# Kernel tuning notes

Measured on AMD Instinct MI355X. Metric: run time of the kernel, lower is better.

The kernel has to match this reference:

```python
import jax, jax.numpy as jnp
import numpy as np

CONF_THRESH = 0.3
NMS_THRESH = 0.5
TOP_K = 64
VAR = (0.1, 0.2)  # standard SSD decode variances


def setup_inputs() -> dict:
    key = jax.random.key(0)
    k1, k2, k3 = jax.random.split(key, 3)
    B, A, C = 16, 16384, 81
    loc = jax.random.normal(k1, (B, A, 4), jnp.float32)
    conf = jax.random.normal(k2, (B, A, C), jnp.float32)
    anchors = jax.random.uniform(k3, (A, 4), jnp.float32)  # cxcywh in [0,1]
    return {"loc": loc, "conf": conf, "anchors": anchors}


def _decode(loc, anchors):
    # SSD-style decode: loc [A,4] offsets, anchors [A,4] cxcywh -> corners [A,4]
    cxcy = anchors[:, :2] + loc[:, :2] * VAR[0] * anchors[:, 2:]
    wh = anchors[:, 2:] * jnp.exp(loc[:, 2:] * VAR[1])
    tl = cxcy - wh * 0.5
    return jnp.concatenate([tl, tl + wh], axis=1)


def _iou(box, boxes):
    # box [4], boxes [A,4] in corner format
    tl = jnp.maximum(box[:2], boxes[:, :2])
    br = jnp.minimum(box[2:], boxes[:, 2:])
    wh = jnp.clip(br - tl, 0.0)
    inter = wh[:, 0] * wh[:, 1]
    a1 = (box[2] - box[0]) * (box[3] - box[1])
    a2 = (boxes[:, 2] - boxes[:, 0]) * (boxes[:, 3] - boxes[:, 1])
    return inter / (a1 + a2 - inter)


def _nms(boxes, scores):
    # greedy NMS for one (batch, class) lane; boxes [A,4], scores [A]
    s0 = jnp.where(scores > CONF_THRESH, scores, -1.0)

    def step(s, _):
        i = jnp.argmax(s)
        sc = s[i]
        box = boxes[i]
        keep = sc > 0.0  # -1 means masked/suppressed; valid scores > conf_thresh > 0
        supp = jnp.where(_iou(box, boxes) > NMS_THRESH, -1.0, s).at[i].set(-1.0)
        s_next = jnp.where(keep, supp, s)
        row = jnp.where(keep, jnp.concatenate([sc[None], box]),
                        jnp.zeros((5,), s.dtype))
        return s_next, row

    _, rows = jax.lax.scan(step, s0, None, length=TOP_K)
    return rows  # [TOP_K, 5] = (score, x1, y1, x2, y2), zero-padded


def reference(loc, conf, anchors):
    conf = jax.nn.sigmoid(conf)                      # [B,A,C]
    boxes = jax.vmap(_decode, in_axes=(0, None))(loc, anchors)  # [B,A,4]
    scores = jnp.swapaxes(conf, 1, 2)                # [B,C,A]
    per_class = jax.vmap(_nms, in_axes=(None, 0))    # over classes
    out = jax.vmap(per_class)(boxes, scores)         # [B,C,TOP_K,5]
    return out
```

## Files before the change

### kernel.cpp

```cpp
#include <hip/hip_runtime.h>
#include <math.h>

constexpr int B_N  = 16;
constexpr int A_N  = 16384;
constexpr int C_N  = 81;
constexpr int TOPK = 64;
constexpr int DNT  = 256;
constexpr int NBINS = 232;
constexpr int CAP   = 512;
constexpr unsigned BIN_BASE = 0x3E99u;

constexpr int TA   = 64;
constexpr int TNT  = 256;
constexpr int TILE_ELEMS = TA * C_N;

__global__ __launch_bounds__(DNT) void decode_kernel(const float4* __restrict__ loc,
                                                     const float4* __restrict__ anch,
                                                     float4* __restrict__ boxes) {
    int i = blockIdx.x * DNT + threadIdx.x;
    int a = i & (A_N - 1);
    float4 l  = loc[i];
    float4 an = anch[a];
    float cx = an.x + (l.x * 0.1f) * an.z;
    float cy = an.y + (l.y * 0.1f) * an.w;
    float w  = an.z * expf(l.z * 0.2f);
    float h  = an.w * expf(l.w * 0.2f);
    float x1 = cx - w * 0.5f;
    float y1 = cy - h * 0.5f;
    boxes[i] = make_float4(x1, y1, x1 + w, y1 + h);
}

__global__ __launch_bounds__(TNT) void sigT_kernel(const float* __restrict__ conf,
                                                   float* __restrict__ scoresT) {
    __shared__ float tile[C_N][TA + 1];

    const int a0 = blockIdx.x * TA;
    const int b  = blockIdx.y;
    const int t  = threadIdx.x;

    const float* src = conf + ((size_t)b * A_N + a0) * C_N;
#pragma unroll
    for (int i = 0; i < (TILE_ELEMS + TNT - 1) / TNT; ++i) {
        int idx = i * TNT + t;
        if (idx < TILE_ELEMS) {
            float x = src[idx];
            int al = idx / C_N;
            int cc = idx - al * C_N;
            tile[cc][al] = 1.0f / (1.0f + expf(-x));
        }
    }
    __syncthreads();
    float* dst = scoresT + (size_t)b * C_N * A_N + a0;
#pragma unroll
    for (int i = 0; i < (TILE_ELEMS + TNT - 1) / TNT; ++i) {
        int idx = i * TNT + t;
        if (idx < TILE_ELEMS) {
            int cc = idx >> 6;
            int al = idx & (TA - 1);
            dst[(size_t)cc * A_N + al] = tile[cc][al];
        }
    }
}

template <bool TRANSPOSED>
__global__ __launch_bounds__(64, 4) void nms_kernel(const float* __restrict__ conf,
                                                    const float* __restrict__ scoresT,
                                                    const float4* __restrict__ boxes,
                                                    float* __restrict__ out) {
    __shared__ int hist[NBINS];
    __shared__ unsigned long long cand[CAP];
    __shared__ int s_cnt;

    const int c    = blockIdx.x;
    const int b    = blockIdx.y;
    const int lane = threadIdx.x;

    for (int i = lane; i < NBINS; i += 64) hist[i] = 0;
    __syncthreads();

    const float4* bptr = boxes + (size_t)b * A_N;
    const float4* sptr = (const float4*)(scoresT + ((size_t)b * C_N + c) * A_N);
    const float*  cptr = conf + (size_t)b * A_N * C_N + c;
    float* optr = out + ((size_t)(b * C_N + c)) * TOPK * 5;

    for (int i = 0; i < A_N / 256; ++i) {
        float s[4];
        if (TRANSPOSED) {
            float4 s4 = sptr[lane + 64 * i];
            s[0] = s4.x; s[1] = s4.y; s[2] = s4.z; s[3] = s4.w;
        } else {
            int a0 = 4 * (lane + 64 * i);
#pragma unroll
            for (int q = 0; q < 4; ++q) {
                float x = cptr[(size_t)(a0 + q) * C_N];
                s[q] = 1.0f / (1.0f + expf(-x));
            }
        }
#pragma unroll
        for (int q = 0; q < 4; ++q) {
            if (s[q] > 0.3f) {
                unsigned u = __float_as_uint(s[q]);
                int bin = (int)(u >> 16) - (int)BIN_BASE;
                bin = bin < 0 ? 0 : (bin > NBINS - 1 ? NBINS - 1 : bin);
                atomicAdd(&hist[bin], 1);
            }
        }
    }
    __syncthreads();

    float rx1 = 0.f, ry1 = 0.f, rx2 = 0.f, ry2 = 0.f, rar = 0.f;
    int acc = 0, kout = 0;

    int bin_hi = NBINS;
    for (;;) {
        int lo = bin_hi, tot = 0;
        while (lo > 0) {
            int cnt = hist[lo - 1];
            if (tot + cnt > CAP) {
                if (tot == 0) { lo--; }
                break;
            }
            tot += cnt; lo--;
        }
        const int bin_lo = lo;
        if (bin_lo == bin_hi) break;
        if (lane == 0) s_cnt = 0;
        __syncthreads();

        for (int i = 0; i < A_N / 256; ++i) {
            float s[4];
            if (TRANSPOSED) {
                float4 s4 = sptr[lane + 64 * i];
                s[0] = s4.x; s[1] = s4.y; s[2] = s4.z; s[3] = s4.w;
            } else {
                int a0 = 4 * (lane + 64 * i);
#pragma unroll
                for (int q = 0; q < 4; ++q) {
                    float x = cptr[(size_t)(a0 + q) * C_N];
                    s[q] = 1.0f / (1.0f + expf(-x));
                }
            }
#pragma unroll
            for (int q = 0; q < 4; ++q) {
                if (s[q] > 0.3f) {
                    unsigned u = __float_as_uint(s[q]);
                    int bin = (int)(u >> 16) - (int)BIN_BASE;
                    bin = bin < 0 ? 0 : (bin > NBINS - 1 ? NBINS - 1 : bin);
                    if (bin >= bin_lo && bin < bin_hi) {
                        int slot = atomicAdd(&s_cnt, 1);
                        if (slot < CAP) {
                            unsigned a = (unsigned)(4 * (lane + 64 * i) + q);
                            cand[slot] = ((unsigned long long)u << 32) | (unsigned)(~a);
                        }
                    }
                }
            }
        }
        __syncthreads();
        int C = s_cnt; if (C > CAP) C = CAP;

        if (C > 0) {
            unsigned long long key[8];
#pragma unroll
            for (int r = 0; r < 8; ++r) {
                int sidx = r * 64 + lane;
                key[r] = (sidx < C) ? cand[sidx] : 0ull;
            }
#pragma unroll
            for (int k = 2; k <= CAP; k <<= 1) {
#pragma unroll
                for (int j = k >> 1; j > 0; j >>= 1) {
                    if (j >= 64) {
                        int jr = j >> 6;
#pragma unroll
                        for (int r = 0; r < 8; ++r) {
                            int rp = r ^ jr;
                            if (rp > r) {
                                int e = r * 64 + lane;
                                bool up = ((e & k) == 0);
                                unsigned long long va = key[r], vb = key[rp];
                                bool sw = up ? (va < vb) : (va > vb);
                                if (sw) { key[r] = vb; key[rp] = va; }
                            }
                        }
                    } else {
#pragma unroll
                        for (int r = 0; r < 8; ++r) {
                            int e = r * 64 + lane;
                            bool up    = ((e & k) == 0);
                            bool isLow = ((lane & j) == 0);
                            unsigned long long va = key[r];
                            unsigned long long vb = __shfl_xor(va, j, 64);
                            bool keepMax = (up == isLow);
                            key[r] = keepMax ? (va > vb ? va : vb)
                                             : (va < vb ? va : vb);
                        }
                    }
                }
            }
            __syncthreads();
#pragma unroll
            for (int r = 0; r < 8; ++r) cand[r * 64 + lane] = key[r];
            __syncthreads();

            int t = 0;
            unsigned long long k0 = cand[0];
            float4 cb = bptr[(int)(~(unsigned)k0)];
            while (t < C) {
                unsigned long long nk = 0ull;
                float4 nb = cb;
                if (t + 1 < C) {
                    nk = cand[t + 1];
                    nb = bptr[(int)(~(unsigned)nk)];
                }
                float sc = __uint_as_float((unsigned)(k0 >> 32));
                float ca = (cb.z - cb.x) * (cb.w - cb.y);
                bool over = false;
                if (lane < acc) {
                    float tlx = fmaxf(rx1, cb.x);
                    float tly = fmaxf(ry1, cb.y);
                    float brx = fminf(rx2, cb.z);
                    float bry = fminf(ry2, cb.w);
                    float iw  = fmaxf(brx - tlx, 0.0f);
                    float ih  = fmaxf(bry - tly, 0.0f);
                    float inter = iw * ih;
                    float iou = inter / (rar + ca - inter);
                    over = iou > 0.5f;
                }
                if (!__any(over)) {
                    if (lane == acc) { rx1 = cb.x; ry1 = cb.y; rx2 = cb.z; ry2 = cb.w; rar = ca; }
                    if (lane == 0) {
                        float* o = optr + (size_t)kout * 5;
                        o[0] = sc; o[1] = cb.x; o[2] = cb.y; o[3] = cb.z; o[4] = cb.w;
                    }
                    acc++; kout++;
                    if (acc == TOPK) break;
                }
                ++t; k0 = nk; cb = nb;
            }
        }
        if (acc == TOPK) break;
        bin_hi = bin_lo;
    }

    {
        float* o  = optr + (size_t)kout * 5;
        int   rem = (TOPK - kout) * 5;
        for (int t = lane; t < rem; t += 64) o[t] = 0.0f;
    }
}

extern "C" void kernel_launch(void* const* d_in, const int* in_sizes, int n_in,
                              void* d_out, int out_size, void* d_ws, size_t ws_size,
                              hipStream_t stream) {
    const float* loc     = (const float*)d_in[0];
    const float* conf    = (const float*)d_in[1];
    const float* anchors = (const float*)d_in[2];
    float* out = (float*)d_out;

    const size_t boxes_bytes  = (size_t)B_N * A_N * sizeof(float4);
    const size_t scores_bytes = (size_t)B_N * C_N * A_N * sizeof(float);

    float4* boxes = (float4*)d_ws;

    decode_kernel<<<(B_N * A_N) / DNT, DNT, 0, stream>>>(
        (const float4*)loc, (const float4*)anchors, boxes);

    if (ws_size >= boxes_bytes + scores_bytes) {
        float* scoresT = (float*)((char*)d_ws + boxes_bytes);
        sigT_kernel<<<dim3(A_N / TA, B_N), TNT, 0, stream>>>(conf, scoresT);
        nms_kernel<true><<<dim3(C_N, B_N), 64, 0, stream>>>(conf, scoresT, boxes, out);
    } else {
        nms_kernel<false><<<dim3(C_N, B_N), 64, 0, stream>>>(conf, nullptr, boxes, out);
    }
}
```

Measured before the change: 267.5 us.

## Split histogram into separate wide kernel, vectorize transpose stores, stage candidate boxes in LDS

Moves the per-(batch,class) score histogram out of the 64-thread NMS kernel into its own 256-thread kernel that writes histograms to workspace, so the scan over 16K scores runs with more parallelism. The transpose kernel now uses a 128-anchor tile stored anchor-major with padding and writes float4 stores. The NMS kernel gathers candidate boxes into shared memory in parallel before the serial greedy loop, so that loop no longer waits on a dependent global load each step. This costs an extra kernel launch, a global histogram round trip and more LDS per block, and the fast path now also needs workspace room for the histograms.

Result: faster. 254.3 us (-4.9%).

```diff
diff --git a/kernel.cpp b/kernel.cpp
--- a/kernel.cpp
+++ b/kernel.cpp
@@ -10,9 +10,13 @@
 constexpr int CAP   = 512;
 constexpr unsigned BIN_BASE = 0x3E99u;
 
-constexpr int TA   = 64;
+constexpr int TA   = 128;
+constexpr int TPAD = 85;
 constexpr int TNT  = 256;
 constexpr int TILE_ELEMS = TA * C_N;
+constexpr int TILE_F4    = (TA / 4) * C_N;
+
+constexpr int HNT = 256;
 
 __global__ __launch_bounds__(DNT) void decode_kernel(const float4* __restrict__ loc,
                                                      const float4* __restrict__ anch,
@@ -32,7 +36,7 @@
 
 __global__ __launch_bounds__(TNT) void sigT_kernel(const float* __restrict__ conf,
                                                    float* __restrict__ scoresT) {
-    __shared__ float tile[C_N][TA + 1];
+    __shared__ float tile[TA][TPAD];
 
     const int a0 = blockIdx.x * TA;
     const int b  = blockIdx.y;
@@ -43,59 +47,41 @@
     for (int i = 0; i < (TILE_ELEMS + TNT - 1) / TNT; ++i) {
         int idx = i * TNT + t;
         if (idx < TILE_ELEMS) {
-            float x = src[idx];
-            int al = idx / C_N;
-            int cc = idx - al * C_N;
-            tile[cc][al] = 1.0f / (1.0f + expf(-x));
+            float x  = src[idx];
+            int   al = idx / C_N;
+            int   cc = idx - al * C_N;
+            tile[al][cc] = 1.0f / (1.0f + expf(-x));
         }
     }
     __syncthreads();
     float* dst = scoresT + (size_t)b * C_N * A_N + a0;
 #pragma unroll
-    for (int i = 0; i < (TILE_ELEMS + TNT - 1) / TNT; ++i) {
-        int idx = i * TNT + t;
-        if (idx < TILE_ELEMS) {
-            int cc = idx >> 6;
-            int al = idx & (TA - 1);
-            dst[(size_t)cc * A_N + al] = tile[cc][al];
-        }
-    }
-}
-
-template <bool TRANSPOSED>
-__global__ __launch_bounds__(64, 4) void nms_kernel(const float* __restrict__ conf,
-                                                    const float* __restrict__ scoresT,
-                                                    const float4* __restrict__ boxes,
-                                                    float* __restrict__ out) {
+    for (int i = 0; i < (TILE_F4 + TNT - 1) / TNT; ++i) {
+        int idx4 = i * TNT + t;
+        if (idx4 < TILE_F4) {
+            int cc  = idx4 >> 5;
+            int al4 = idx4 & 31;
+            float4 v;
+            v.x = tile[al4 * 4 + 0][cc];
+            v.y = tile[al4 * 4 + 1][cc];
+            v.z = tile[al4 * 4 + 2][cc];
+            v.w = tile[al4 * 4 + 3][cc];
+            ((float4*)(dst + (size_t)cc * A_N))[al4] = v;
+        }
+    }
+}
+
+__global__ __launch_bounds__(HNT) void hist_kernel(const float* __restrict__ scoresT,
+                                                   int* __restrict__ ghist) {
     __shared__ int hist[NBINS];
-    __shared__ unsigned long long cand[CAP];
-    __shared__ int s_cnt;
-
-    const int c    = blockIdx.x;
-    const int b    = blockIdx.y;
-    const int lane = threadIdx.x;
-
-    for (int i = lane; i < NBINS; i += 64) hist[i] = 0;
+    const int bc = blockIdx.x;
+    const int t  = threadIdx.x;
+    for (int i = t; i < NBINS; i += HNT) hist[i] = 0;
     __syncthreads();
-
-    const float4* bptr = boxes + (size_t)b * A_N;
-    const float4* sptr = (const float4*)(scoresT + ((size_t)b * C_N + c) * A_N);
-    const float*  cptr = conf + (size_t)b * A_N * C_N + c;
-    float* optr = out + ((size_t)(b * C_N + c)) * TOPK * 5;
-
-    for (int i = 0; i < A_N / 256; ++i) {
-        float s[4];
-        if (TRANSPOSED) {
-            float4 s4 = sptr[lane + 64 * i];
-            s[0] = s4.x; s[1] = s4.y; s[2] = s4.z; s[3] = s4.w;
-        } else {
-            int a0 = 4 * (lane + 64 * i);
-#pragma unroll
-            for (int q = 0; q < 4; ++q) {
-                float x = cptr[(size_t)(a0 + q) * C_N];
-                s[q] = 1.0f / (1.0f + expf(-x));
-            }
-        }
+    const float4* sptr = (const float4*)(scoresT + (size_t)bc * A_N);
+    for (int i = 0; i < A_N / 4 / HNT; ++i) {
+        float4 s4 = sptr[t + HNT * i];
+        float s[4] = {s4.x, s4.y, s4.z, s4.w};
 #pragma unroll
         for (int q = 0; q < 4; ++q) {
             if (s[q] > 0.3f) {
@@ -103,6 +89,52 @@
                 int bin = (int)(u >> 16) - (int)BIN_BASE;
                 bin = bin < 0 ? 0 : (bin > NBINS - 1 ? NBINS - 1 : bin);
                 atomicAdd(&hist[bin], 1);
+            }
+        }
+    }
+    __syncthreads();
+    int* g = ghist + (size_t)bc * NBINS;
+    for (int i = t; i < NBINS; i += HNT) g[i] = hist[i];
+}
+
+template <bool TRANSPOSED>
+__global__ __launch_bounds__(64, 4) void nms_kernel(const float* __restrict__ conf,
+                                                    const float* __restrict__ scoresT,
+                                                    const int* __restrict__ ghist,
+                                                    const float4* __restrict__ boxes,
+                                                    float* __restrict__ out) {
+    __shared__ int hist[NBINS];
+    __shared__ unsigned long long cand[CAP];
+    __shared__ float4 cbox[CAP];
+    __shared__ int s_cnt;
+
+    const int c    = blockIdx.x;
+    const int b    = blockIdx.y;
+    const int lane = threadIdx.x;
+
+    const float4* bptr = boxes + (size_t)b * A_N;
+    const float4* sptr = (const float4*)(scoresT + ((size_t)b * C_N + c) * A_N);
+    const float*  cptr = conf + (size_t)b * A_N * C_N + c;
+    float* optr = out + ((size_t)(b * C_N + c)) * TOPK * 5;
+
+    if (TRANSPOSED) {
+        const int* g = ghist + (size_t)(b * C_N + c) * NBINS;
+        for (int i = lane; i < NBINS; i += 64) hist[i] = g[i];
+    } else {
+        for (int i = lane; i < NBINS; i += 64) hist[i] = 0;
+        __syncthreads();
+        for (int i = 0; i < A_N / 256; ++i) {
+            int a0 = 4 * (lane + 64 * i);
+#pragma unroll
+            for (int q = 0; q < 4; ++q) {
+                float x = cptr[(size_t)(a0 + q) * C_N];
+                float s = 1.0f / (1.0f + expf(-x));
+                if (s > 0.3f) {
+                    unsigned u = __float_as_uint(s);
+                    int bin = (int)(u >> 16) - (int)BIN_BASE;
+                    bin = bin < 0 ? 0 : (bin > NBINS - 1 ? NBINS - 1 : bin);
+                    atomicAdd(&hist[bin], 1);
+                }
             }
         }
     }
@@ -203,16 +235,23 @@
             for (int r = 0; r < 8; ++r) cand[r * 64 + lane] = key[r];
             __syncthreads();
 
+#pragma unroll
+            for (int r = 0; r < 8; ++r) {
+                int e = r * 64 + lane;
+                if (e < C) {
+                    int idx = (int)(~(unsigned)cand[e]);
+                    cbox[e] = bptr[idx];
+                }
+            }
+            __syncthreads();
+
             int t = 0;
             unsigned long long k0 = cand[0];
-            float4 cb = bptr[(int)(~(unsigned)k0)];
+            float4 cb = cbox[0];
             while (t < C) {
                 unsigned long long nk = 0ull;
                 float4 nb = cb;
-                if (t + 1 < C) {
-                    nk = cand[t + 1];
-                    nb = bptr[(int)(~(unsigned)nk)];
-                }
+                if (t + 1 < C) { nk = cand[t + 1]; nb = cbox[t + 1]; }
                 float sc = __uint_as_float((unsigned)(k0 >> 32));
                 float ca = (cb.z - cb.x) * (cb.w - cb.y);
                 bool over = false;
@@ -260,17 +299,20 @@
 
     const size_t boxes_bytes  = (size_t)B_N * A_N * sizeof(float4);
     const size_t scores_bytes = (size_t)B_N * C_N * A_N * sizeof(float);
+    const size_t hist_bytes   = (size_t)B_N * C_N * NBINS * sizeof(int);
 
     float4* boxes = (float4*)d_ws;
 
     decode_kernel<<<(B_N * A_N) / DNT, DNT, 0, stream>>>(
         (const float4*)loc, (const float4*)anchors, boxes);
 
-    if (ws_size >= boxes_bytes + scores_bytes) {
+    if (ws_size >= boxes_bytes + scores_bytes + hist_bytes) {
         float* scoresT = (float*)((char*)d_ws + boxes_bytes);
+        int*   ghist   = (int*)((char*)d_ws + boxes_bytes + scores_bytes);
         sigT_kernel<<<dim3(A_N / TA, B_N), TNT, 0, stream>>>(conf, scoresT);
-        nms_kernel<true><<<dim3(C_N, B_N), 64, 0, stream>>>(conf, scoresT, boxes, out);
+        hist_kernel<<<dim3(B_N * C_N), HNT, 0, stream>>>(scoresT, ghist);
+        nms_kernel<true><<<dim3(C_N, B_N), 64, 0, stream>>>(conf, scoresT, ghist, boxes, out);
     } else {
-        nms_kernel<false><<<dim3(C_N, B_N), 64, 0, stream>>>(conf, nullptr, boxes, out);
-    }
-}
+        nms_kernel<false><<<dim3(C_N, B_N), 64, 0, stream>>>(conf, nullptr, nullptr, boxes, out);
+    }
+}
```
